# Optimization experiments

Measured on AMD Instinct MI355X. Metric: run time of the kernel, lower is better.

The kernel has to match this reference:

```python
import jax, jax.numpy as jnp
import numpy as np

B, S, D = 16, 1024, 384
H, DH = 6, 64  # head_dim = hidden // heads


def setup_inputs() -> dict:
    key = jax.random.key(0)
    ks = jax.random.split(key, 9)
    std = 0.02
    return {
        "x": jax.random.normal(ks[0], (B, S, D), jnp.float32),
        "Wq": jax.random.normal(ks[1], (H, D, DH), jnp.float32) * std,
        "bq": jax.random.normal(ks[2], (H, DH), jnp.float32) * std,
        "Wk": jax.random.normal(ks[3], (H, D, DH), jnp.float32) * std,
        "bk": jax.random.normal(ks[4], (H, DH), jnp.float32) * std,
        "Wv": jax.random.normal(ks[5], (H, D, DH), jnp.float32) * std,
        "bv": jax.random.normal(ks[6], (H, DH), jnp.float32) * std,
        "Wo": jax.random.normal(ks[7], (D, D), jnp.float32) * std,  # [out, in] like nn.Linear
        "bo": jax.random.normal(ks[8], (D,), jnp.float32) * std,
    }


def reference(x, Wq, bq, Wk, bk, Wv, bv, Wo, bo):
    # Per-head q/k/v projections (stacked over heads h)
    q = jnp.einsum("bsd,hde->bhse", x, Wq) + bq[None, :, None, :]
    k = jnp.einsum("bsd,hde->bhse", x, Wk) + bk[None, :, None, :]
    v = jnp.einsum("bsd,hde->bhse", x, Wv) + bv[None, :, None, :]
    # Explicit softmax attention (dropout prob = 0.0 in config)
    scores = jnp.einsum("bhse,bhte->bhst", q, k) / jnp.sqrt(jnp.float32(DH))
    probs = jax.nn.softmax(scores, axis=-1)
    ctx = jnp.einsum("bhst,bhte->bhse", probs, v)  # [B,H,S,DH]
    # Concat heads along last dim: [B,S,H*DH]
    concat = jnp.transpose(ctx, (0, 2, 1, 3)).reshape(B, S, H * DH)
    # Output projection (nn.Linear: y = x @ W^T + b)
    out = jnp.einsum("bsd,ed->bse", concat, Wo) + bo
    return out
```

## Files before the change

### kernel.cpp

```cpp
#include <hip/hip_runtime.h>
#include <hip/hip_bf16.h>

typedef __attribute__((ext_vector_type(8))) short short8;
typedef __attribute__((ext_vector_type(4))) short short4v;
typedef __attribute__((ext_vector_type(4))) float float4v;
typedef __attribute__((ext_vector_type(4))) int int4v;

#define MFMA16(a,b,c) __builtin_amdgcn_mfma_f32_16x16x32_bf16((a),(b),(c),0,0,0)
#define EXP2(x) __builtin_amdgcn_exp2f(x)

static constexpr int Bz = 16, Sq = 1024, Dm = 384, Hh = 6, Dh = 64;
static constexpr int Mtok = Bz * Sq;
static constexpr int NQKV = 1152;

__device__ __forceinline__ short f2bf(float f) {
  union { float f; unsigned u; } v; v.f = f;
  unsigned r = v.u + 0x7fffu + ((v.u >> 16) & 1u);
  return (short)(r >> 16);
}

__device__ __forceinline__ unsigned cvtpk(float a, float b) {
  unsigned d;
  asm("v_cvt_pk_bf16_f32 %0, %1, %2" : "=v"(d) : "v"(a), "v"(b));
  return d;
}

__device__ __forceinline__ void gload16(const void* src, void* lds) {
  __builtin_amdgcn_global_load_lds(
      (const __attribute__((address_space(1))) unsigned int*)src,
      (__attribute__((address_space(3))) unsigned int*)lds, 16, 0, 0);
}

__device__ __forceinline__ int vperm(int s) {
  return (s & ~31) | ((s & 12) << 1) | ((s & 16) >> 2) | (s & 3);
}

__global__ __launch_bounds__(256) void conv_x(const float* __restrict__ x,
                                              short* __restrict__ xb) {
  const int i = (blockIdx.x * 256 + threadIdx.x) * 8;
  float4v v0 = *(const float4v*)(x + i);
  float4v v1 = *(const float4v*)(x + i + 4);
  short8 o;
  o[0] = f2bf(v0[0]); o[1] = f2bf(v0[1]); o[2] = f2bf(v0[2]); o[3] = f2bf(v0[3]);
  o[4] = f2bf(v1[0]); o[5] = f2bf(v1[1]); o[6] = f2bf(v1[2]); o[7] = f2bf(v1[3]);
  *(short8*)(xb + i) = o;
}

__global__ __launch_bounds__(256) void conv_w(const float* __restrict__ Wq,
                                              const float* __restrict__ Wk,
                                              const float* __restrict__ Wv,
                                              const float* __restrict__ bq,
                                              const float* __restrict__ bk,
                                              const float* __restrict__ bv,
                                              const float* __restrict__ Wo,
                                              short* __restrict__ Wt,
                                              float* __restrict__ bias,
                                              short* __restrict__ Wob) {
  const float SCL = 0.125f * 1.44269504088896340736f;
  const int i = blockIdx.x * 256 + threadIdx.x;
  const int NW = NQKV * Dm;
  if (i < NW) {
    const int c = i / Dm, d = i % Dm;
    const int p = c / 384, rr = c % 384;
    const int h = rr >> 6, dh = rr & 63;
    const float* W = (p == 0) ? Wq : ((p == 1) ? Wk : Wv);
    float w = W[(h * Dm + d) * Dh + dh];
    if (p == 0) w *= SCL;
    Wt[c * Dm + d] = f2bf(w);
  } else if (i < NW + NQKV) {
    const int c = i - NW;
    const int p = c / 384, rr = c % 384;
    const int h = rr >> 6, dh = rr & 63;
    const float* bb = (p == 0) ? bq : ((p == 1) ? bk : bv);
    float b = bb[h * Dh + dh];
    if (p == 0) b *= SCL;
    bias[c] = b;
  } else if (i < NW + NQKV + Dm * Dm) {
    const int j = i - NW - NQKV;
    Wob[j] = f2bf(Wo[j]);
  }
}


__global__ __launch_bounds__(256) void qkv_gemm(const short* __restrict__ Xb,
                                                const short* __restrict__ Wt,
                                                const float* __restrict__ bias,
                                                short* __restrict__ qkv,
                                                short* __restrict__ vt) {
  __shared__ char smem[49152];
  const int tid = threadIdx.x;
  const int wave = tid >> 6, lane = tid & 63;
  const int r = lane & 15, g = lane >> 4;
  const int wr = wave >> 1, wc = wave & 1;

  const int flat = blockIdx.x;
  const int w = (flat & 7) * 144 + (flat >> 3);
  const int bx = w % 9, by = w / 9;
  const int bm0 = by * 128, bn0 = bx * 128;
  const int m0 = bm0 + wr * 64, n0 = bn0 + wc * 64;

  float bv_n[4];
#pragma unroll
  for (int ni = 0; ni < 4; ++ni) bv_n[ni] = bias[n0 + ni * 16 + r];
  asm volatile("s_waitcnt vmcnt(0)" ::: "memory");

  const char *aSrc0, *aSrc1, *bSrc0, *bSrc1;
  {
    const int o0 = tid * 16, o1 = 4096 + tid * 16;
    const int lr0 = o0 >> 7, cb0 = (o0 & 127) ^ ((lr0 & 7) << 4);
    const int lr1 = o1 >> 7, cb1 = (o1 & 127) ^ ((lr1 & 7) << 4);
    const int m_0 = 2 * lr0 + (cb0 >> 6), kb0 = cb0 & 63;
    const int m_1 = 2 * lr1 + (cb1 >> 6), kb1 = cb1 & 63;
    aSrc0 = (const char*)(Xb + (bm0 + m_0) * Dm) + kb0;
    aSrc1 = (const char*)(Xb + (bm0 + m_1) * Dm) + kb1;
    bSrc0 = (const char*)(Wt + (bn0 + m_0) * Dm) + kb0;
    bSrc1 = (const char*)(Wt + (bn0 + m_1) * Dm) + kb1;
  }
  auto stage = [&](int t, int buf) {
    char* base = smem + buf * 16384;
    const int kb = t * 64;
    gload16(aSrc0 + kb, base + wave * 1024);
    gload16(aSrc1 + kb, base + 4096 + wave * 1024);
    gload16(bSrc0 + kb, base + 8192 + wave * 1024);
    gload16(bSrc1 + kb, base + 12288 + wave * 1024);
  };

  int aOff[4], bOff[4];
#pragma unroll
  for (int i = 0; i < 4; ++i) {
    const int m = wr * 64 + i * 16 + r;
    const int lr = m >> 1;
    aOff[i] = lr * 128 + ((((m & 1) << 6) | (16 * g)) ^ ((lr & 7) << 4));
    const int n = wc * 64 + i * 16 + r;
    const int lrn = n >> 1;
    bOff[i] = 8192 + lrn * 128 + ((((n & 1) << 6) | (16 * g)) ^ ((lrn & 7) << 4));
  }

  float4v acc[4][4] = {};
  auto compute = [&](int buf) {
    const char* sb = smem + buf * 16384;
    short8 a[4], b[4];
#pragma unroll
    for (int i = 0; i < 4; ++i) a[i] = *(const short8*)(sb + aOff[i]);
#pragma unroll
    for (int i = 0; i < 4; ++i) b[i] = *(const short8*)(sb + bOff[i]);
#pragma unroll
    for (int mi = 0; mi < 4; ++mi)
#pragma unroll
      for (int ni = 0; ni < 4; ++ni)
        acc[mi][ni] = MFMA16(a[mi], b[ni], acc[mi][ni]);
  };

  stage(0, 0);
  stage(1, 1);
  stage(2, 2);
#pragma unroll 1
  for (int t = 0; t < 10; ++t) {
    asm volatile("s_waitcnt vmcnt(8)" ::: "memory");
    __builtin_amdgcn_s_barrier();
    compute(t % 3);
    __builtin_amdgcn_s_barrier();
    if (t < 9) stage(t + 3, t % 3);
  }
  asm volatile("s_waitcnt vmcnt(4)" ::: "memory");
  __builtin_amdgcn_s_barrier();
  compute(1);
  asm volatile("s_waitcnt vmcnt(0)" ::: "memory");
  __builtin_amdgcn_s_barrier();
  compute(2);

#pragma unroll
  for (int ni = 0; ni < 4; ++ni) {
    const int col = n0 + ni * 16 + r;
    const int p = col / 384, rr2 = col % 384;
    const int h = rr2 >> 6, dh = rr2 & 63;
    const float bv = bv_n[ni];
#pragma unroll
    for (int mi = 0; mi < 4; ++mi) {
#pragma unroll
      for (int rp = 0; rp < 2; ++rp) {
        const unsigned u = cvtpk(acc[mi][ni][2 * rp] + bv,
                                 acc[mi][ni][2 * rp + 1] + bv);
        const short lo = (short)u, hi = (short)(u >> 16);
        const int mg = m0 + mi * 16 + 4 * g + 2 * rp;
        if (p < 2) {
          qkv[mg * NQKV + col] = lo;
          qkv[(mg + 1) * NQKV + col] = hi;
        } else {
          const int bb = mg >> 10, s = mg & 1023;
          const int sp = vperm(s);
          short* vp = vt + ((bb * Hh + h) * Dh + dh) * Sq;
          vp[sp] = lo;
          vp[sp + 1] = hi;
        }
      }
    }
  }
}

__global__ __launch_bounds__(256) void attn(const short* __restrict__ qkv,
                                            const short* __restrict__ vt,
                                            short* __restrict__ ctx) {
  __shared__ char smem[32768];
  const int tid = threadIdx.x;
  const int wave = tid >> 6, lane = tid & 63;
  const int r = lane & 15, g = lane >> 4;
  const int xr = (r & 7) << 4;
  const int flat = blockIdx.x;
  const int w = (flat & 7) * 96 + (flat >> 3);
  const int qb = w & 7, bh = w >> 3;
  const int b = bh / Hh, h = bh % Hh;
  const int tok0 = b * Sq;
  const int qw = qb * 128 + wave * 32;

  short8 qf[2][2];
#pragma unroll
  for (int f = 0; f < 2; ++f) {
    const short* qp = qkv + (tok0 + qw + 16 * f + r) * NQKV + h * Dh;
    qf[f][0] = *(const short8*)(qp + 8 * g);
    qf[f][1] = *(const short8*)(qp + 32 + 8 * g);
  }
  asm volatile("s_waitcnt vmcnt(0)" ::: "memory");

  const short* kg = qkv + tok0 * NQKV + 384 + h * Dh;
  const short* vg = vt + (b * Hh + h) * Dh * Sq;

  const int o0 = wave * 2048 + lane * 16;
  const int row0 = o0 >> 7, cb0 = (o0 & 127) ^ ((row0 & 7) << 4);
  const int o1 = o0 + 1024;
  const int row1 = o1 >> 7, cb1 = (o1 & 127) ^ ((row1 & 7) << 4);

#define STAGE(T, BUFSEL)                                                        \
  {                                                                             \
    char* kb_ = smem + (BUFSEL) * 16384;                                        \
    const int kv_ = (T) * 64;                                                   \
    gload16((const char*)(kg + (kv_ + row0) * NQKV) + cb0, kb_ + wave * 2048);  \
    gload16((const char*)(vg + row0 * Sq + kv_) + cb0, kb_ + 8192 + wave * 2048);\
    gload16((const char*)(kg + (kv_ + row1) * NQKV) + cb1, kb_ + wave * 2048 + 1024);\
    gload16((const char*)(vg + row1 * Sq + kv_) + cb1, kb_ + 8192 + wave * 2048 + 1024);\
  }

  int kOff[4][2], vOff[4][2];
#pragma unroll
  for (int kt = 0; kt < 4; ++kt)
#pragma unroll
    for (int c = 0; c < 2; ++c)
      kOff[kt][c] = (16 * kt + r) * 128 + ((64 * c + 16 * g) ^ xr);
#pragma unroll
  for (int d = 0; d < 4; ++d)
#pragma unroll
    for (int h2 = 0; h2 < 2; ++h2)
      vOff[d][h2] = (16 * d + r) * 128 + ((64 * h2 + 16 * g) ^ xr);

  float4v acc[4][2] = {};
  float lsum[2] = {0.f, 0.f};

  auto compute = [&](int bufsel) {
    const char* kb = smem + bufsel * 16384;
    const char* vb = kb + 8192;
    short8 kf[4][2];
#pragma unroll
    for (int kt = 0; kt < 4; ++kt) {
      kf[kt][0] = *(const short8*)(kb + kOff[kt][0]);
      kf[kt][1] = *(const short8*)(kb + kOff[kt][1]);
    }
    short8 vf[4][2];
#pragma unroll
    for (int d = 0; d < 4; ++d)
#pragma unroll
      for (int h2 = 0; h2 < 2; ++h2)
        vf[d][h2] = *(const short8*)(vb + vOff[d][h2]);
    float4v s[4][2];
    __builtin_amdgcn_s_setprio(1);
#pragma unroll
    for (int kt = 0; kt < 4; ++kt)
#pragma unroll
      for (int f = 0; f < 2; ++f) {
        float4v z = {};
        z = MFMA16(kf[kt][0], qf[f][0], z);
        z = MFMA16(kf[kt][1], qf[f][1], z);
        s[kt][f] = z;
      }
    __builtin_amdgcn_s_setprio(0);
    short8 pa[2][2];
#pragma unroll
    for (int f = 0; f < 2; ++f) {
      float ps = 0.f;
#pragma unroll
      for (int h2 = 0; h2 < 2; ++h2) {
        float e0[4], e1[4];
#pragma unroll
        for (int j = 0; j < 4; ++j) {
          e0[j] = EXP2(s[2 * h2][f][j]);
          e1[j] = EXP2(s[2 * h2 + 1][f][j]);
          ps += e0[j] + e1[j];
        }
        int4v wv;
        wv[0] = (int)cvtpk(e0[0], e0[1]);
        wv[1] = (int)cvtpk(e0[2], e0[3]);
        wv[2] = (int)cvtpk(e1[0], e1[1]);
        wv[3] = (int)cvtpk(e1[2], e1[3]);
        pa[f][h2] = __builtin_bit_cast(short8, wv);
      }
      lsum[f] += ps;
    }
    __builtin_amdgcn_s_setprio(1);
#pragma unroll
    for (int d = 0; d < 4; ++d)
#pragma unroll
      for (int f = 0; f < 2; ++f) {
        acc[d][f] = MFMA16(pa[f][0], vf[d][0], acc[d][f]);
        acc[d][f] = MFMA16(pa[f][1], vf[d][1], acc[d][f]);
      }
    __builtin_amdgcn_s_setprio(0);
  };

  STAGE(0, 0)
  STAGE(1, 1)
#pragma unroll 1
  for (int t = 0; t < 15; ++t) {
    asm volatile("s_waitcnt vmcnt(4)" ::: "memory");
    __builtin_amdgcn_s_barrier();
    compute(t & 1);
    __builtin_amdgcn_s_barrier();
    if (t < 14) STAGE(t + 2, t & 1)
  }
  asm volatile("s_waitcnt vmcnt(0)" ::: "memory");
  __builtin_amdgcn_s_barrier();
  compute(1);

#pragma unroll
  for (int f = 0; f < 2; ++f) {
    lsum[f] += __shfl_xor(lsum[f], 16);
    lsum[f] += __shfl_xor(lsum[f], 32);
  }
#pragma unroll
  for (int f = 0; f < 2; ++f) {
    float il[4];
#pragma unroll
    for (int reg = 0; reg < 4; ++reg) il[reg] = 1.f / __shfl(lsum[f], 4 * g + reg);
#pragma unroll
    for (int d = 0; d < 4; ++d) {
      short* cp = ctx + (tok0 + qw + 16 * f + 4 * g) * Dm + h * Dh + 16 * d + r;
#pragma unroll
      for (int reg = 0; reg < 4; ++reg)
        cp[reg * Dm] = f2bf(acc[d][f][reg] * il[reg]);
    }
  }
}

__global__ __launch_bounds__(256) void out_gemm(const short* __restrict__ ctx,
                                                const short* __restrict__ Wob,
                                                const float* __restrict__ bo,
                                                float* __restrict__ out) {
  __shared__ char smem[49152];
  const int tid = threadIdx.x;
  const int wave = tid >> 6, lane = tid & 63;
  const int r = lane & 15, g = lane >> 4;
  const int wr = wave >> 1, wc = wave & 1;

  const int flat = blockIdx.x;
  const int w = (flat & 7) * 48 + (flat >> 3);
  const int bx = w % 3, by = w / 3;
  const int bm0 = by * 128, bn0 = bx * 128;
  const int m0 = bm0 + wr * 64, n0 = bn0 + wc * 64;

  float bv_n[4];
#pragma unroll
  for (int ni = 0; ni < 4; ++ni) bv_n[ni] = bo[n0 + ni * 16 + r];
  asm volatile("s_waitcnt vmcnt(0)" ::: "memory");

  const char *aSrc0, *aSrc1, *bSrc0, *bSrc1;
  {
    const int o0 = tid * 16, o1 = 4096 + tid * 16;
    const int lr0 = o0 >> 7, cb0 = (o0 & 127) ^ ((lr0 & 7) << 4);
    const int lr1 = o1 >> 7, cb1 = (o1 & 127) ^ ((lr1 & 7) << 4);
    const int m_0 = 2 * lr0 + (cb0 >> 6), kb0 = cb0 & 63;
    const int m_1 = 2 * lr1 + (cb1 >> 6), kb1 = cb1 & 63;
    aSrc0 = (const char*)(ctx + (bm0 + m_0) * Dm) + kb0;
    aSrc1 = (const char*)(ctx + (bm0 + m_1) * Dm) + kb1;
    bSrc0 = (const char*)(Wob + (bn0 + m_0) * Dm) + kb0;
    bSrc1 = (const char*)(Wob + (bn0 + m_1) * Dm) + kb1;
  }
  auto stage = [&](int t, int buf) {
    char* base = smem + buf * 16384;
    const int kb = t * 64;
    gload16(aSrc0 + kb, base + wave * 1024);
    gload16(aSrc1 + kb, base + 4096 + wave * 1024);
    gload16(bSrc0 + kb, base + 8192 + wave * 1024);
    gload16(bSrc1 + kb, base + 12288 + wave * 1024);
  };

  int aOff[4], bOff[4];
#pragma unroll
  for (int i = 0; i < 4; ++i) {
    const int m = wr * 64 + i * 16 + r;
    const int lr = m >> 1;
    aOff[i] = lr * 128 + ((((m & 1) << 6) | (16 * g)) ^ ((lr & 7) << 4));
    const int n = wc * 64 + i * 16 + r;
    const int lrn = n >> 1;
    bOff[i] = 8192 + lrn * 128 + ((((n & 1) << 6) | (16 * g)) ^ ((lrn & 7) << 4));
  }

  float4v acc[4][4] = {};
  auto compute = [&](int buf) {
    const char* sb = smem + buf * 16384;
    short8 a[4], b[4];
#pragma unroll
    for (int i = 0; i < 4; ++i) a[i] = *(const short8*)(sb + aOff[i]);
#pragma unroll
    for (int i = 0; i < 4; ++i) b[i] = *(const short8*)(sb + bOff[i]);
#pragma unroll
    for (int mi = 0; mi < 4; ++mi)
#pragma unroll
      for (int ni = 0; ni < 4; ++ni)
        acc[mi][ni] = MFMA16(a[mi], b[ni], acc[mi][ni]);
  };

  stage(0, 0);
  stage(1, 1);
  stage(2, 2);
#pragma unroll 1
  for (int t = 0; t < 10; ++t) {
    asm volatile("s_waitcnt vmcnt(8)" ::: "memory");
    __builtin_amdgcn_s_barrier();
    compute(t % 3);
    __builtin_amdgcn_s_barrier();
    if (t < 9) stage(t + 3, t % 3);
  }
  asm volatile("s_waitcnt vmcnt(4)" ::: "memory");
  __builtin_amdgcn_s_barrier();
  compute(1);
  asm volatile("s_waitcnt vmcnt(0)" ::: "memory");
  __builtin_amdgcn_s_barrier();
  compute(2);

#pragma unroll
  for (int ni = 0; ni < 4; ++ni) {
    const int col = n0 + ni * 16 + r;
    const float bv = bv_n[ni];
#pragma unroll
    for (int mi = 0; mi < 4; ++mi) {
#pragma unroll
      for (int reg = 0; reg < 4; ++reg) {
        const int mg = m0 + mi * 16 + 4 * g + reg;
        out[mg * Dm + col] = acc[mi][ni][reg] + bv;
      }
    }
  }
}

extern "C" void kernel_launch(void* const* d_in, const int* in_sizes, int n_in,
                              void* d_out, int out_size, void* d_ws, size_t ws_size,
                              hipStream_t stream) {
  const float* x  = (const float*)d_in[0];
  const float* Wq = (const float*)d_in[1];
  const float* bq = (const float*)d_in[2];
  const float* Wk = (const float*)d_in[3];
  const float* bk = (const float*)d_in[4];
  const float* Wv = (const float*)d_in[5];
  const float* bv = (const float*)d_in[6];
  const float* Wo = (const float*)d_in[7];
  const float* bo = (const float*)d_in[8];
  float* out = (float*)d_out;

  char* ws = (char*)d_ws;
  short* Xb   = (short*)(ws);
  short* Wt   = (short*)(ws + 12582912);
  float* bias = (float*)(ws + 13467648);
  short* Wob  = (short*)(ws + 13472256);
  short* qkv  = (short*)(ws + 13767168);
  short* vt   = (short*)(ws + 51515904);
  short* ctx  = (short*)(ws + 64098816);

  conv_x<<<Mtok * Dm / (256 * 8), 256, 0, stream>>>(x, Xb);
  conv_w<<<(NQKV * Dm + NQKV + Dm * Dm + 255) / 256, 256, 0, stream>>>(
      Wq, Wk, Wv, bq, bk, bv, Wo, Wt, bias, Wob);
  qkv_gemm<<<1152, 256, 0, stream>>>(Xb, Wt, bias, qkv, vt);
  attn<<<768, 256, 0, stream>>>(qkv, vt, ctx);
  out_gemm<<<384, 256, 0, stream>>>(ctx, Wob, bo, out);
}
```

Baseline: 100.4 us.

## Halve attention query tile, reshape GEMM staging to one barrier, pack V stores

Attention blocks now handle 64 queries (16 per wave) instead of 128. That doubles the grid to 1536 blocks, cuts register use, and adds a launch-bounds occupancy hint, at the cost of loading each K/V tile twice as often. Both GEMMs now keep two stages in flight and refill the third buffer right after compute, dropping the second barrier per iteration. The V-transpose epilogue writes two bf16 values as one 32-bit store.

```diff
diff --git a/kernel.cpp b/kernel.cpp
--- a/kernel.cpp
+++ b/kernel.cpp
@@ -81,7 +81,6 @@
   }
 }
 
-
 __global__ __launch_bounds__(256) void qkv_gemm(const short* __restrict__ Xb,
                                                 const short* __restrict__ Wt,
                                                 const float* __restrict__ bias,
@@ -153,14 +152,12 @@
 
   stage(0, 0);
   stage(1, 1);
-  stage(2, 2);
 #pragma unroll 1
   for (int t = 0; t < 10; ++t) {
-    asm volatile("s_waitcnt vmcnt(8)" ::: "memory");
+    asm volatile("s_waitcnt vmcnt(4)" ::: "memory");
     __builtin_amdgcn_s_barrier();
     compute(t % 3);
-    __builtin_amdgcn_s_barrier();
-    if (t < 9) stage(t + 3, t % 3);
+    stage(t + 2, (t + 2) % 3);
   }
   asm volatile("s_waitcnt vmcnt(4)" ::: "memory");
   __builtin_amdgcn_s_barrier();
@@ -181,45 +178,39 @@
       for (int rp = 0; rp < 2; ++rp) {
         const unsigned u = cvtpk(acc[mi][ni][2 * rp] + bv,
                                  acc[mi][ni][2 * rp + 1] + bv);
-        const short lo = (short)u, hi = (short)(u >> 16);
         const int mg = m0 + mi * 16 + 4 * g + 2 * rp;
         if (p < 2) {
-          qkv[mg * NQKV + col] = lo;
-          qkv[(mg + 1) * NQKV + col] = hi;
+          qkv[mg * NQKV + col] = (short)u;
+          qkv[(mg + 1) * NQKV + col] = (short)(u >> 16);
         } else {
           const int bb = mg >> 10, s = mg & 1023;
           const int sp = vperm(s);
           short* vp = vt + ((bb * Hh + h) * Dh + dh) * Sq;
-          vp[sp] = lo;
-          vp[sp + 1] = hi;
+          *(unsigned*)(vp + sp) = u;
         }
       }
     }
   }
 }
 
-__global__ __launch_bounds__(256) void attn(const short* __restrict__ qkv,
-                                            const short* __restrict__ vt,
-                                            short* __restrict__ ctx) {
+__global__ __launch_bounds__(256, 5) void attn(const short* __restrict__ qkv,
+                                               const short* __restrict__ vt,
+                                               short* __restrict__ ctx) {
   __shared__ char smem[32768];
   const int tid = threadIdx.x;
   const int wave = tid >> 6, lane = tid & 63;
   const int r = lane & 15, g = lane >> 4;
   const int xr = (r & 7) << 4;
   const int flat = blockIdx.x;
-  const int w = (flat & 7) * 96 + (flat >> 3);
-  const int qb = w & 7, bh = w >> 3;
+  const int w = (flat & 7) * 192 + (flat >> 3);
+  const int qb = w & 15, bh = w >> 4;
   const int b = bh / Hh, h = bh % Hh;
   const int tok0 = b * Sq;
-  const int qw = qb * 128 + wave * 32;
-
-  short8 qf[2][2];
-#pragma unroll
-  for (int f = 0; f < 2; ++f) {
-    const short* qp = qkv + (tok0 + qw + 16 * f + r) * NQKV + h * Dh;
-    qf[f][0] = *(const short8*)(qp + 8 * g);
-    qf[f][1] = *(const short8*)(qp + 32 + 8 * g);
-  }
+  const int qw = qb * 64 + wave * 16;
+
+  const short* qp = qkv + (tok0 + qw + r) * NQKV + h * Dh;
+  const short8 qf0 = *(const short8*)(qp + 8 * g);
+  const short8 qf1 = *(const short8*)(qp + 32 + 8 * g);
   asm volatile("s_waitcnt vmcnt(0)" ::: "memory");
 
   const short* kg = qkv + tok0 * NQKV + 384 + h * Dh;
@@ -252,8 +243,8 @@
     for (int h2 = 0; h2 < 2; ++h2)
       vOff[d][h2] = (16 * d + r) * 128 + ((64 * h2 + 16 * g) ^ xr);
 
-  float4v acc[4][2] = {};
-  float lsum[2] = {0.f, 0.f};
+  float4v acc[4] = {};
+  float lsum = 0.f;
 
   auto compute = [&](int bufsel) {
     const char* kb = smem + bufsel * 16384;
@@ -270,48 +261,41 @@
 #pragma unroll
       for (int h2 = 0; h2 < 2; ++h2)
         vf[d][h2] = *(const short8*)(vb + vOff[d][h2]);
-    float4v s[4][2];
+    float4v s[4];
     __builtin_amdgcn_s_setprio(1);
 #pragma unroll
-    for (int kt = 0; kt < 4; ++kt)
-#pragma unroll
-      for (int f = 0; f < 2; ++f) {
-        float4v z = {};
-        z = MFMA16(kf[kt][0], qf[f][0], z);
-        z = MFMA16(kf[kt][1], qf[f][1], z);
-        s[kt][f] = z;
+    for (int kt = 0; kt < 4; ++kt) {
+      float4v z = {};
+      z = MFMA16(kf[kt][0], qf0, z);
+      z = MFMA16(kf[kt][1], qf1, z);
+      s[kt] = z;
+    }
+    __builtin_amdgcn_s_setprio(0);
+    short8 pa[2];
+    float ps = 0.f;
+#pragma unroll
+    for (int h2 = 0; h2 < 2; ++h2) {
+      float e0[4], e1[4];
+#pragma unroll
+      for (int j = 0; j < 4; ++j) {
+        e0[j] = EXP2(s[2 * h2][j]);
+        e1[j] = EXP2(s[2 * h2 + 1][j]);
+        ps += e0[j] + e1[j];
       }
-    __builtin_amdgcn_s_setprio(0);
-    short8 pa[2][2];
-#pragma unroll
-    for (int f = 0; f < 2; ++f) {
-      float ps = 0.f;
-#pragma unroll
-      for (int h2 = 0; h2 < 2; ++h2) {
-        float e0[4], e1[4];
-#pragma unroll
-        for (int j = 0; j < 4; ++j) {
-          e0[j] = EXP2(s[2 * h2][f][j]);
-          e1[j] = EXP2(s[2 * h2 + 1][f][j]);
-          ps += e0[j] + e1[j];
-        }
-        int4v wv;
-        wv[0] = (int)cvtpk(e0[0], e0[1]);
-        wv[1] = (int)cvtpk(e0[2], e0[3]);
-        wv[2] = (int)cvtpk(e1[0], e1[1]);
-        wv[3] = (int)cvtpk(e1[2], e1[3]);
-        pa[f][h2] = __builtin_bit_cast(short8, wv);
-      }
-      lsum[f] += ps;
-    }
+      int4v wv;
+      wv[0] = (int)cvtpk(e0[0], e0[1]);
+      wv[1] = (int)cvtpk(e0[2], e0[3]);
+      wv[2] = (int)cvtpk(e1[0], e1[1]);
+      wv[3] = (int)cvtpk(e1[2], e1[3]);
+      pa[h2] = __builtin_bit_cast(short8, wv);
+    }
+    lsum += ps;
     __builtin_amdgcn_s_setprio(1);
 #pragma unroll
-    for (int d = 0; d < 4; ++d)
-#pragma unroll
-      for (int f = 0; f < 2; ++f) {
-        acc[d][f] = MFMA16(pa[f][0], vf[d][0], acc[d][f]);
-        acc[d][f] = MFMA16(pa[f][1], vf[d][1], acc[d][f]);
-      }
+    for (int d = 0; d < 4; ++d) {
+      acc[d] = MFMA16(pa[0], vf[d][0], acc[d]);
+      acc[d] = MFMA16(pa[1], vf[d][1], acc[d]);
+    }
     __builtin_amdgcn_s_setprio(0);
   };
 
@@ -329,23 +313,17 @@
   __builtin_amdgcn_s_barrier();
   compute(1);
 
-#pragma unroll
-  for (int f = 0; f < 2; ++f) {
-    lsum[f] += __shfl_xor(lsum[f], 16);
-    lsum[f] += __shfl_xor(lsum[f], 32);
-  }
-#pragma unroll
-  for (int f = 0; f < 2; ++f) {
-    float il[4];
-#pragma unroll
-    for (int reg = 0; reg < 4; ++reg) il[reg] = 1.f / __shfl(lsum[f], 4 * g + reg);
-#pragma unroll
-    for (int d = 0; d < 4; ++d) {
-      short* cp = ctx + (tok0 + qw + 16 * f + 4 * g) * Dm + h * Dh + 16 * d + r;
-#pragma unroll
-      for (int reg = 0; reg < 4; ++reg)
-        cp[reg * Dm] = f2bf(acc[d][f][reg] * il[reg]);
-    }
+  lsum += __shfl_xor(lsum, 16);
+  lsum += __shfl_xor(lsum, 32);
+  float il[4];
+#pragma unroll
+  for (int reg = 0; reg < 4; ++reg) il[reg] = 1.f / __shfl(lsum, 4 * g + reg);
+#pragma unroll
+  for (int d = 0; d < 4; ++d) {
+    short* cp = ctx + (tok0 + qw + 4 * g) * Dm + h * Dh + 16 * d + r;
+#pragma unroll
+    for (int reg = 0; reg < 4; ++reg)
+      cp[reg * Dm] = f2bf(acc[d][reg] * il[reg]);
   }
 }
 
@@ -419,14 +397,12 @@
 
   stage(0, 0);
   stage(1, 1);
-  stage(2, 2);
 #pragma unroll 1
   for (int t = 0; t < 10; ++t) {
-    asm volatile("s_waitcnt vmcnt(8)" ::: "memory");
+    asm volatile("s_waitcnt vmcnt(4)" ::: "memory");
     __builtin_amdgcn_s_barrier();
     compute(t % 3);
-    __builtin_amdgcn_s_barrier();
-    if (t < 9) stage(t + 3, t % 3);
+    stage(t + 2, (t + 2) % 3);
   }
   asm volatile("s_waitcnt vmcnt(4)" ::: "memory");
   __builtin_amdgcn_s_barrier();
@@ -477,6 +453,6 @@
   conv_w<<<(NQKV * Dm + NQKV + Dm * Dm + 255) / 256, 256, 0, stream>>>(
       Wq, Wk, Wv, bq, bk, bv, Wo, Wt, bias, Wob);
   qkv_gemm<<<1152, 256, 0, stream>>>(Xb, Wt, bias, qkv, vt);
-  attn<<<768, 256, 0, stream>>>(qkv, vt, ctx);
+  attn<<<1536, 256, 0, stream>>>(qkv, vt, ctx);
   out_gemm<<<384, 256, 0, stream>>>(ctx, Wob, bo, out);
 }
```

Result: slower. 106.6 us (+6.2%).
